# Optimization experiments

Measured on AMD Instinct MI355X. Metric: run time of the kernel, lower is better.

The kernel has to match this reference:

```python
import jax, jax.numpy as jnp
import numpy as np

FEAT_STRIDE = 16
SCALES = np.array([8.0, 16.0, 32.0])
RATIOS = np.array([0.5, 1.0, 2.0])
PRE_NMS_TOP_N = 6000
POST_NMS_TOP_N = 300
NMS_THRESH = 0.7


def _whctrs(anchor):
    w = anchor[2] - anchor[0] + 1.0
    h = anchor[3] - anchor[1] + 1.0
    cx = anchor[0] + 0.5 * (w - 1.0)
    cy = anchor[1] + 0.5 * (h - 1.0)
    return w, h, cx, cy


def _mkanchors(ws, hs, cx, cy):
    return np.stack([cx - 0.5 * (ws - 1.0), cy - 0.5 * (hs - 1.0),
                     cx + 0.5 * (ws - 1.0), cy + 0.5 * (hs - 1.0)], axis=1)


def generate_anchors(base_size=16, ratios=RATIOS, scales=SCALES):
    base = np.array([0.0, 0.0, base_size - 1.0, base_size - 1.0])
    w, h, cx, cy = _whctrs(base)
    size = w * h
    ws = np.round(np.sqrt(size / ratios))
    hs = np.round(ws * ratios)
    ratio_anchors = _mkanchors(ws, hs, cx, cy)
    out = []
    for a in ratio_anchors:
        w, h, cx, cy = _whctrs(a)
        out.append(_mkanchors(w * scales, h * scales, cx, cy))
    return np.vstack(out)  # (A=9, 4)


def setup_inputs():
    key = jax.random.key(0)
    k1, k2 = jax.random.split(key)
    B, A, H, W = 8, 9, 152, 152
    scores_in = jax.random.normal(k1, (B, 2 * A, H, W), jnp.float32)
    bbox_deltas = 0.5 * jax.random.normal(k2, (B, 4 * A, H, W), jnp.float32)
    im_info = jnp.tile(jnp.array([[H * FEAT_STRIDE, W * FEAT_STRIDE, 1.0]], jnp.float32), (B, 1))
    anchors = jnp.asarray(generate_anchors(), jnp.float32)
    return {"scores_in": scores_in, "bbox_deltas": bbox_deltas, "im_info": im_info, "anchors": anchors}


def bbox_transform_inv(boxes, deltas):
    w = boxes[..., 2] - boxes[..., 0] + 1.0
    h = boxes[..., 3] - boxes[..., 1] + 1.0
    cx = boxes[..., 0] + 0.5 * w
    cy = boxes[..., 1] + 0.5 * h
    dx, dy, dw, dh = deltas[..., 0], deltas[..., 1], deltas[..., 2], deltas[..., 3]
    pcx = dx * w + cx
    pcy = dy * h + cy
    pw = jnp.exp(dw) * w
    ph = jnp.exp(dh) * h
    return jnp.stack([pcx - 0.5 * pw, pcy - 0.5 * ph, pcx + 0.5 * pw, pcy + 0.5 * ph], axis=-1)


def clip_boxes(boxes, im_info):
    wmax = im_info[:, None, 1] - 1.0  # x bound, per image
    hmax = im_info[:, None, 0] - 1.0  # y bound
    x1 = jnp.minimum(jnp.maximum(boxes[..., 0], 0.0), wmax)
    y1 = jnp.minimum(jnp.maximum(boxes[..., 1], 0.0), hmax)
    x2 = jnp.minimum(jnp.maximum(boxes[..., 2], 0.0), wmax)
    y2 = jnp.minimum(jnp.maximum(boxes[..., 3], 0.0), hmax)
    return jnp.stack([x1, y1, x2, y2], axis=-1)


def nms_indices(boxes, thresh, max_out):
    # boxes: (N, 4), sorted by score descending. Greedy NMS -> up to max_out indices, -1 padded.
    x1, y1, x2, y2 = boxes[:, 0], boxes[:, 1], boxes[:, 2], boxes[:, 3]
    areas = (x2 - x1 + 1.0) * (y2 - y1 + 1.0)
    N = boxes.shape[0]

    def body(i, carry):
        suppressed, keep = carry
        idx = jnp.argmax(~suppressed)  # first surviving box = highest remaining score
        valid = ~suppressed[idx]
        keep = keep.at[i].set(jnp.where(valid, idx.astype(jnp.int32), -1))
        xx1 = jnp.maximum(x1[idx], x1)
        yy1 = jnp.maximum(y1[idx], y1)
        xx2 = jnp.minimum(x2[idx], x2)
        yy2 = jnp.minimum(y2[idx], y2)
        inter = jnp.maximum(xx2 - xx1 + 1.0, 0.0) * jnp.maximum(yy2 - yy1 + 1.0, 0.0)
        iou = inter / (areas[idx] + areas - inter)
        suppressed = jnp.where(valid, suppressed | (iou > thresh), suppressed)
        return suppressed, keep

    _, keep = jax.lax.fori_loop(0, max_out, body,
                                (jnp.zeros(N, bool), jnp.full(max_out, -1, jnp.int32)))
    return keep


def _forward(scores_in, bbox_deltas, im_info, anchors):
    B, _, H, W = scores_in.shape
    A = anchors.shape[0]
    # fg objectness scores: channels [A:2A] -> (B, K*A) in (row, col, anchor) order
    scores = scores_in[:, A:].transpose(0, 2, 3, 1).reshape(B, -1)
    deltas = bbox_deltas.transpose(0, 2, 3, 1).reshape(B, -1, 4)
    sx = (jnp.arange(W) * FEAT_STRIDE).astype(jnp.float32)
    sy = (jnp.arange(H) * FEAT_STRIDE).astype(jnp.float32)
    gx, gy = jnp.meshgrid(sx, sy)  # (H, W)
    shifts = jnp.stack([gx.ravel(), gy.ravel(), gx.ravel(), gy.ravel()], axis=1)  # (K, 4)
    all_anchors = (anchors[None, :, :] + shifts[:, None, :]).reshape(-1, 4)  # (K*A, 4)
    proposals = bbox_transform_inv(all_anchors[None], deltas)  # (B, K*A, 4)
    proposals = clip_boxes(proposals, im_info)
    _, order = jax.lax.top_k(scores, PRE_NMS_TOP_N)  # descending, == sorted order truncated
    props_top = jnp.take_along_axis(proposals, order[..., None], axis=1)  # (B, PRE, 4)
    keep = jax.vmap(lambda b: nms_indices(b, NMS_THRESH, POST_NMS_TOP_N))(props_top)  # (B, POST)
    valid = keep >= 0
    sel = jnp.take_along_axis(props_top, jnp.maximum(keep, 0)[..., None], axis=1)
    sel = jnp.where(valid[..., None], sel, 0.0)
    batch_col = jnp.broadcast_to(jnp.arange(B, dtype=jnp.float32)[:, None, None],
                                 (B, POST_NMS_TOP_N, 1))
    return jnp.concatenate([batch_col, sel], axis=2)  # (B, POST, 5)


def reference(scores_in, bbox_deltas, im_info, anchors):
    return _forward(scores_in, bbox_deltas, im_info, anchors)
```

## Files before the change

### kernel.cpp

```cpp
#include <hip/hip_runtime.h>
#include <stdint.h>

#define H_ 152
#define W_ 152
#define A_ 9
#define HW_ (H_ * W_)
#define N_ (HW_ * A_)
#define B_ 8
#define PRE_TOP 6000
#define POST_TOP 300
#define NBUCK 4096
#define NFINE 32768
#define CAND_CAP 8192
#define NMS_TH 0.7f
#define CNT_STRIDE 32
#define RTILE 512

#define OFF_HIST    0
#define OFF_SSUF    131072
#define OFF_CNT     262144
#define OFF_CAND    263168
#define OFF_GROUP   787456
#define OFF_BOXES   1311744
#define OFF_BALL    2079744
#define WS_NEED     (2079744ull + 26615808ull)


__device__ __forceinline__ unsigned fkey(float f) {
    unsigned u = __float_as_uint(f);
    return (u & 0x80000000u) ? ~u : (u | 0x80000000u);
}

__device__ __forceinline__ bool sup_test(float ax1, float ay1, float ax2, float ay2, float aar,
                                         float bx1, float by1, float bx2, float by2, float bar) {
    float xx1 = fmaxf(ax1, bx1);
    float yy1 = fmaxf(ay1, by1);
    float xx2 = fminf(ax2, bx2);
    float yy2 = fminf(ay2, by2);
    float iw = fmaxf(xx2 - xx1 + 1.0f, 0.0f);
    float ih = fmaxf(yy2 - yy1 + 1.0f, 0.0f);
    float inter = __fmul_rn(iw, ih);
    float iou = inter / (aar + bar - inter);
    return iou > NMS_TH;
}

__device__ __forceinline__ float4 decode_box(float an0, float an1, float an2, float an3,
                                             float sx, float sy,
                                             float dx, float dy, float dw, float dh,
                                             float wmax, float hmax) {
    float ax1 = an0 + sx;
    float ay1 = an1 + sy;
    float ax2 = an2 + sx;
    float ay2 = an3 + sy;
    float ww = ax2 - ax1 + 1.0f;
    float hh = ay2 - ay1 + 1.0f;
    float ctx = ax1 + 0.5f * ww;
    float cty = ay1 + 0.5f * hh;
    float pcx = __fadd_rn(__fmul_rn(dx, ww), ctx);
    float pcy = __fadd_rn(__fmul_rn(dy, hh), cty);
    float pw = __fmul_rn(expf(dw), ww);
    float ph = __fmul_rn(expf(dh), hh);
    float x1 = pcx - 0.5f * pw;
    float y1 = pcy - 0.5f * ph;
    float x2 = pcx + 0.5f * pw;
    float y2 = pcy + 0.5f * ph;
    x1 = fminf(fmaxf(x1, 0.0f), wmax);
    y1 = fminf(fmaxf(y1, 0.0f), hmax);
    x2 = fminf(fmaxf(x2, 0.0f), wmax);
    y2 = fminf(fmaxf(y2, 0.0f), hmax);
    return make_float4(x1, y1, x2, y2);
}


__global__ void zero2_k(unsigned* __restrict__ base, unsigned* __restrict__ p2) {
    const int n1 = 263168 / 4;
    const int n2 = 768000 / 4;
    int i = blockIdx.x * blockDim.x + threadIdx.x;
    int st = gridDim.x * blockDim.x;
    for (int k = i; k < n1 + n2; k += st) {
        if (k < n1) base[k] = 0u;
        else p2[k - n1] = 0u;
    }
}

__global__ void decode_all_k(const float* __restrict__ deltas,
                             const float* __restrict__ anchors,
                             const float* __restrict__ im_info,
                             float4* __restrict__ ball) {
    int ba = blockIdx.y;
    int b = ba / A_, a = ba - (ba / A_) * A_;
    int pix = blockIdx.x * blockDim.x + threadIdx.x;
    if (pix >= HW_) return;
    const float* db = deltas + ((size_t)b * 36 + 4 * a) * HW_;
    float dx = db[pix];
    float dy = db[pix + HW_];
    float dw = db[pix + 2 * HW_];
    float dh = db[pix + 3 * HW_];
    float an0 = anchors[a * 4 + 0];
    float an1 = anchors[a * 4 + 1];
    float an2 = anchors[a * 4 + 2];
    float an3 = anchors[a * 4 + 3];
    float hmax = im_info[b * 3 + 0] - 1.0f;
    float wmax = im_info[b * 3 + 1] - 1.0f;
    int w = pix % W_, h = pix / W_;
    float sx = (float)(w * 16), sy = (float)(h * 16);
    ball[(size_t)b * N_ + a * HW_ + pix] =
        decode_box(an0, an1, an2, an3, sx, sy, dx, dy, dw, dh, wmax, hmax);
}

__global__ void hist_k(const float* __restrict__ scores, unsigned* __restrict__ hist) {
    __shared__ unsigned lh[NBUCK];
    int b = blockIdx.y;
    for (int i = threadIdx.x; i < NBUCK; i += blockDim.x) lh[i] = 0;
    __syncthreads();
    const float4* sb = (const float4*)(scores + ((size_t)b * 18 + A_) * HW_);
    const int N4 = N_ / 4;
    int stride = gridDim.x * blockDim.x;
    for (int e = blockIdx.x * blockDim.x + threadIdx.x; e < N4; e += stride) {
        float4 v = sb[e];
        atomicAdd(&lh[fkey(v.x) >> 20], 1u);
        atomicAdd(&lh[fkey(v.y) >> 20], 1u);
        atomicAdd(&lh[fkey(v.z) >> 20], 1u);
        atomicAdd(&lh[fkey(v.w) >> 20], 1u);
    }
    __syncthreads();
    for (int i = threadIdx.x; i < NBUCK; i += blockDim.x) {
        unsigned v = lh[i];
        if (v) atomicAdd(&hist[b * NBUCK + i], v);
    }
}

__global__ void scan_k(const unsigned* __restrict__ hist, unsigned* __restrict__ bucketT) {
    __shared__ unsigned ps[1024];
    int b = blockIdx.x, t = threadIdx.x;
    const unsigned* hb = hist + b * NBUCK;
    unsigned c0 = hb[4095 - (4 * t + 0)];
    unsigned c1 = hb[4095 - (4 * t + 1)];
    unsigned c2 = hb[4095 - (4 * t + 2)];
    unsigned c3 = hb[4095 - (4 * t + 3)];
    unsigned local = c0 + c1 + c2 + c3;
    ps[t] = local;
    __syncthreads();
    for (int off = 1; off < 1024; off <<= 1) {
        unsigned v = (t >= off) ? ps[t - off] : 0u;
        __syncthreads();
        ps[t] += v;
        __syncthreads();
    }
    unsigned incl = ps[t], excl = incl - local;
    if (excl < PRE_TOP && incl >= PRE_TOP) {
        unsigned cum = excl;
        unsigned cc[4] = {c0, c1, c2, c3};
#pragma unroll
        for (int k = 0; k < 4; ++k) {
            cum += cc[k];
            if (cum >= PRE_TOP) { bucketT[b] = (unsigned)(4095 - (4 * t + k)); break; }
        }
    }
    if (t == 1023 && ps[1023] < PRE_TOP) bucketT[b] = 0;
}

__global__ void compact_k(const float* __restrict__ scores, const unsigned* __restrict__ bucketT,
                          unsigned* __restrict__ cnt, uint2* __restrict__ cand) {
    __shared__ unsigned wtot[4], wbase[4];
    __shared__ unsigned blkbase;
    int b = blockIdx.y;
    const float4* sb = (const float4*)(scores + ((size_t)b * 18 + A_) * HW_);
    unsigned T = bucketT[b];
    int lane = threadIdx.x & 63;
    int wid = threadIdx.x >> 6;
    const int N4 = N_ / 4;
    int stride = gridDim.x * blockDim.x;
    int niters = (N4 + stride - 1) / stride;
    unsigned long long lower = (lane == 63) ? 0x7fffffffffffffffull
                                            : ((1ull << lane) - 1ull);
    for (int it = 0; it < niters; ++it) {
        int e = it * stride + blockIdx.x * (int)blockDim.x + (int)threadIdx.x;
        bool p0 = false, p1 = false, p2 = false, p3 = false;
        unsigned k0 = 0, k1 = 0, k2 = 0, k3 = 0;
        if (e < N4) {
            float4 v = sb[e];
            k0 = fkey(v.x); k1 = fkey(v.y); k2 = fkey(v.z); k3 = fkey(v.w);
            p0 = (k0 >> 20) >= T; p1 = (k1 >> 20) >= T;
            p2 = (k2 >> 20) >= T; p3 = (k3 >> 20) >= T;
        }
        unsigned long long m0 = __ballot(p0), m1 = __ballot(p1);
        unsigned long long m2 = __ballot(p2), m3 = __ballot(p3);
        unsigned t0 = (unsigned)__popcll(m0), t1 = (unsigned)__popcll(m1);
        unsigned t2 = (unsigned)__popcll(m2), t3 = (unsigned)__popcll(m3);
        unsigned wtotal = t0 + t1 + t2 + t3;
        if (lane == 0) wtot[wid] = wtotal;
        __syncthreads();
        if (threadIdx.x == 0) {
            unsigned s0 = wtot[0], s1 = wtot[1], s2 = wtot[2], s3 = wtot[3];
            unsigned tot = s0 + s1 + s2 + s3;
            blkbase = tot ? atomicAdd(&cnt[b * CNT_STRIDE], tot) : 0u;
            wbase[0] = 0; wbase[1] = s0; wbase[2] = s0 + s1; wbase[3] = s0 + s1 + s2;
        }
        __syncthreads();
        if (wtotal) {
            unsigned base = blkbase + wbase[wid];
            unsigned o0 = base + (unsigned)__popcll(m0 & lower);
            unsigned o1 = base + t0 + (unsigned)__popcll(m1 & lower);
            unsigned o2 = base + t0 + t1 + (unsigned)__popcll(m2 & lower);
            unsigned o3 = base + t0 + t1 + t2 + (unsigned)__popcll(m3 & lower);
            uint2* cb = cand + (size_t)b * CAND_CAP;
            int e4 = e * 4;
            if (p0 && o0 < CAND_CAP) {
                int a = (e4 + 0) / HW_, pix = (e4 + 0) - a * HW_;
                cb[o0] = make_uint2(k0, (unsigned)(pix * A_ + a));
            }
            if (p1 && o1 < CAND_CAP) {
                int a = (e4 + 1) / HW_, pix = (e4 + 1) - a * HW_;
                cb[o1] = make_uint2(k1, (unsigned)(pix * A_ + a));
            }
            if (p2 && o2 < CAND_CAP) {
                int a = (e4 + 2) / HW_, pix = (e4 + 2) - a * HW_;
                cb[o2] = make_uint2(k2, (unsigned)(pix * A_ + a));
            }
            if (p3 && o3 < CAND_CAP) {
                int a = (e4 + 3) / HW_, pix = (e4 + 3) - a * HW_;
                cb[o3] = make_uint2(k3, (unsigned)(pix * A_ + a));
            }
        }
    }
}

__global__ void __launch_bounds__(1024) finesort_k(const unsigned* __restrict__ cnt,
                                                   uint2* __restrict__ cand,
                                                   unsigned long long* __restrict__ grouped) {
    __shared__ unsigned lh[NFINE];
    __shared__ unsigned ps[1024];
    int b = blockIdx.x, t = threadIdx.x;
    int M = min((int)cnt[b * CNT_STRIDE], CAND_CAP);
    uint2* cb = cand + (size_t)b * CAND_CAP;
    unsigned long long* g = grouped + (size_t)b * CAND_CAP;
    for (int i = t; i < NFINE; i += 1024) lh[i] = 0u;
    __syncthreads();
    for (int i = t; i < M; i += 1024) {
        unsigned key16 = cb[i].x >> 16;
        unsigned f = (key16 >= 32768u) ? (key16 - 32768u) : 0u;
        atomicAdd(&lh[f], 1u);
    }
    __syncthreads();
    unsigned c[32];
    unsigned local = 0;
#pragma unroll
    for (int k = 0; k < 32; ++k) { c[k] = lh[32767 - (32 * t + k)]; local += c[k]; }
    ps[t] = local;
    __syncthreads();
    for (int off = 1; off < 1024; off <<= 1) {
        unsigned v = (t >= off) ? ps[t - off] : 0u;
        __syncthreads();
        ps[t] += v;
        __syncthreads();
    }
    unsigned run = ps[t] - local;
    __syncthreads();
#pragma unroll
    for (int k = 0; k < 32; ++k) {
        lh[32767 - (32 * t + k)] = run;
        run += c[k];
    }
    __syncthreads();
    for (int i = t; i < M; i += 1024) {
        uint2 cd = cb[i];
        unsigned key16 = cd.x >> 16;
        unsigned f = (key16 >= 32768u) ? (key16 - 32768u) : 0u;
        unsigned pos = atomicAdd(&lh[f], 1u);
        if (pos < CAND_CAP)
            g[pos] = ((unsigned long long)cd.x << 32) | (unsigned)(~cd.y);
    }
    __syncthreads();
    ushort* S16 = (ushort*)cb;
    for (int i = t; i < NFINE; i += 1024)
        S16[i] = (ushort)min(lh[i], 65535u);
}

__global__ void __launch_bounds__(256) rank_k(const unsigned* __restrict__ cnt,
                                              const unsigned long long* __restrict__ grouped,
                                              const ushort* __restrict__ S16all,
                                              const float* __restrict__ deltas,
                                              const float* __restrict__ anchors,
                                              const float* __restrict__ im_info,
                                              const float4* __restrict__ ball,
                                              float4* __restrict__ boxes) {
    __shared__ unsigned long long tile[RTILE];
    __shared__ int s_rs, s_re;
    int b = blockIdx.y, t = threadIdx.x;
    int M = min((int)cnt[b * CNT_STRIDE], CAND_CAP);
    int c0 = blockIdx.x * 256;
    if (c0 >= M) return;
    const unsigned long long* g = grouped + (size_t)b * CAND_CAP;
    const ushort* S16 = S16all + (size_t)b * NFINE;
    int i = c0 + t;
    bool valid = i < M;
    unsigned long long comp = valid ? g[i] : 0ull;

    unsigned n = valid ? ~(unsigned)comp : 0u;
    int a = (int)(n % A_);
    int pix = (int)(n / A_);

    float4 pre = make_float4(0.f, 0.f, 0.f, 0.f);
    float dx = 0.f, dy = 0.f, dw = 0.f, dh = 0.f;
    float an0 = 0.f, an1 = 0.f, an2 = 0.f, an3 = 0.f, hmax = 0.f, wmax = 0.f;
    if (ball) {
        if (valid) pre = ball[(size_t)b * N_ + a * HW_ + pix];
    } else if (valid) {
        const float* db = deltas + (size_t)b * 36 * HW_;
        int didx = (4 * a) * HW_ + pix;
        dx = db[didx];
        dy = db[didx + HW_];
        dw = db[didx + 2 * HW_];
        dh = db[didx + 3 * HW_];
        an0 = anchors[a * 4 + 0];
        an1 = anchors[a * 4 + 1];
        an2 = anchors[a * 4 + 2];
        an3 = anchors[a * 4 + 3];
        hmax = im_info[b * 3 + 0] - 1.0f;
        wmax = im_info[b * 3 + 1] - 1.0f;
    }

    unsigned key16 = (unsigned)(comp >> 48);
    int f = (key16 >= 32768u) ? (int)(key16 - 32768u) : 0;
    int bs = 0, be = 0;
    if (valid) {
        bs = (f < 32767) ? min((int)S16[f + 1], M) : 0;
        be = min((int)S16[f], M);
    }
    if (t == 0) {
        unsigned kf = (unsigned)(g[c0] >> 48);
        int bf = (kf >= 32768u) ? (int)(kf - 32768u) : 0;
        int last = min(c0 + 255, M - 1);
        unsigned kl = (unsigned)(g[last] >> 48);
        int bl = (kl >= 32768u) ? (int)(kl - 32768u) : 0;
        s_rs = (bf < 32767) ? min((int)S16[bf + 1], M) : 0;
        s_re = min((int)S16[bl], M);
    }
    __syncthreads();
    int rs = s_rs, re = s_re;
    int cgt = 0;
    for (int tb = rs; tb < re; tb += RTILE) {
        int navail = min(RTILE, re - tb);
        __syncthreads();
        for (int j = t; j < navail; j += 256) tile[j] = g[tb + j];
        __syncthreads();
        if (valid) {
            int lo = max(bs, tb) - tb;
            int hi = min(be, tb + navail) - tb;
            int a0 = 0, a1 = 0, a2 = 0, a3 = 0, a4 = 0, a5 = 0, a6 = 0, a7 = 0;
            int j = lo;
            for (; j + 8 <= hi; j += 8) {
                unsigned long long v0 = tile[j + 0];
                unsigned long long v1 = tile[j + 1];
                unsigned long long v2 = tile[j + 2];
                unsigned long long v3 = tile[j + 3];
                unsigned long long v4 = tile[j + 4];
                unsigned long long v5 = tile[j + 5];
                unsigned long long v6 = tile[j + 6];
                unsigned long long v7 = tile[j + 7];
                a0 += (v0 > comp); a1 += (v1 > comp); a2 += (v2 > comp); a3 += (v3 > comp);
                a4 += (v4 > comp); a5 += (v5 > comp); a6 += (v6 > comp); a7 += (v7 > comp);
            }
            for (; j < hi; ++j) cgt += (tile[j] > comp);
            cgt += (a0 + a1 + a2 + a3) + (a4 + a5 + a6 + a7);
        }
    }
    if (!valid) return;
    int rank = bs + cgt;
    if (rank >= PRE_TOP) return;

    float4 result;
    if (ball) {
        result = pre;
    } else {
        int w = pix % W_, h = pix / W_;
        float sx = (float)(w * 16), sy = (float)(h * 16);
        result = decode_box(an0, an1, an2, an3, sx, sy, dx, dy, dw, dh, wmax, hmax);
    }
    boxes[(size_t)b * PRE_TOP + rank] = result;
}

__global__ void __launch_bounds__(1024) nms_k(const float4* __restrict__ boxes,
                                              float* __restrict__ out) {
    __shared__ float kx1[POST_TOP], ky1[POST_TOP], kx2[POST_TOP], ky2[POST_TOP], kar[POST_TOP];
    __shared__ float gx1[64], gy1[64], gx2[64], gy2[64], gar[64];
    __shared__ unsigned extw[2];
    __shared__ unsigned intraw[128];
    __shared__ unsigned long long s_keep;
    __shared__ int s_base, s_kc, s_done;
    int b = blockIdx.x, t = threadIdx.x;
    if (t == 0) { s_kc = 0; s_done = 0; }
    const float4* bb = boxes + (size_t)b * PRE_TOP;
    const int ngroups = (PRE_TOP + 63) / 64;

    float4 vcur = make_float4(0.f, 0.f, 0.f, 0.f);
    if (t < 64) vcur = bb[t];

    for (int g = 0; g < ngroups; ++g) {
        __syncthreads();
        if (s_done) break;
        int gbase = g * 64;
        int gsz = min(64, PRE_TOP - gbase);
        if (t < gsz) {
            gx1[t] = vcur.x; gy1[t] = vcur.y; gx2[t] = vcur.z; gy2[t] = vcur.w;
            gar[t] = __fmul_rn(vcur.z - vcur.x + 1.0f, vcur.w - vcur.y + 1.0f);
        }
        if (t < 64) {
            int nidx = min(gbase + 64 + t, PRE_TOP - 1);
            vcur = bb[nidx];
        }
        if (t < 2) extw[t] = 0u;
        if (t < 128) intraw[t] = 0u;
        __syncthreads();

        int kc = s_kc;
        {
            int j = t >> 4, sub = t & 15;
            if (j < gsz) {
                float ax1 = gx1[j], ay1 = gy1[j], ax2 = gx2[j], ay2 = gy2[j], aar = gar[j];
                bool any = false;
                for (int kk = sub; kk < kc; kk += 16) {
                    if (sup_test(kx1[kk], ky1[kk], kx2[kk], ky2[kk], kar[kk],
                                 ax1, ay1, ax2, ay2, aar)) { any = true; break; }
                }
                if (any) atomicOr(&extw[j >> 5], 1u << (j & 31));
            }
        }
        for (int p = t; p < 4096; p += 1024) {
            int jj = p >> 6, ll = p & 63;
            if (jj < ll && ll < gsz) {
                if (sup_test(gx1[jj], gy1[jj], gx2[jj], gy2[jj], gar[jj],
                             gx1[ll], gy1[ll], gx2[ll], gy2[ll], gar[ll])) {
                    atomicOr(&intraw[2 * jj + (ll >> 5)], 1u << (ll & 31));
                }
            }
        }
        __syncthreads();

        if (t == 0) {
            unsigned long long ext64 = (unsigned long long)extw[0] |
                                       ((unsigned long long)extw[1] << 32);
            unsigned long long valid = (gsz >= 64) ? ~0ull : ((1ull << gsz) - 1ull);
            unsigned long long alive = (~ext64) & valid;
            unsigned long long keep = 0ull;
            int kcc = s_kc;
            s_base = kcc;
            while (alive && kcc < POST_TOP) {
                int j = __ffsll((long long)alive) - 1;
                keep |= (1ull << j);
                ++kcc;
                unsigned long long row = (unsigned long long)intraw[2 * j] |
                                         ((unsigned long long)intraw[2 * j + 1] << 32);
                alive &= ~row;
                alive &= ~(1ull << j);
            }
            s_keep = keep;
            s_kc = kcc;
            if (kcc >= POST_TOP) s_done = 1;
        }
        __syncthreads();

        if (t < gsz && ((s_keep >> t) & 1ull)) {
            int rank = __popcll(s_keep & ((1ull << t) - 1ull));
            int slot = s_base + rank;
            kx1[slot] = gx1[t]; ky1[slot] = gy1[t];
            kx2[slot] = gx2[t]; ky2[slot] = gy2[t]; kar[slot] = gar[t];
            float* o = out + (size_t)(b * POST_TOP + slot) * 5;
            o[0] = (float)b; o[1] = gx1[t]; o[2] = gy1[t]; o[3] = gx2[t]; o[4] = gy2[t];
        }
    }
    __syncthreads();
    for (int sl = s_kc + t; sl < POST_TOP; sl += 1024) {
        float* o = out + (size_t)(b * POST_TOP + sl) * 5;
        o[0] = (float)b; o[1] = 0.f; o[2] = 0.f; o[3] = 0.f; o[4] = 0.f;
    }
}


extern "C" void kernel_launch(void* const* d_in, const int* in_sizes, int n_in,
                              void* d_out, int out_size, void* d_ws, size_t ws_size,
                              hipStream_t stream) {
    const float* scores  = (const float*)d_in[0];
    const float* deltas  = (const float*)d_in[1];
    const float* im_info = (const float*)d_in[2];
    const float* anchors = (const float*)d_in[3];
    float* out = (float*)d_out;

    unsigned*           hist    = (unsigned*)((char*)d_ws + OFF_HIST);
    unsigned*           cnt     = (unsigned*)((char*)d_ws + OFF_CNT);
    uint2*              cand    = (uint2*)((char*)d_ws + OFF_CAND);
    unsigned long long* grouped = (unsigned long long*)((char*)d_ws + OFF_GROUP);
    float4*             boxes   = (float4*)((char*)d_ws + OFF_BOXES);
    unsigned*           bucketT = cnt + B_ * CNT_STRIDE - 8;

    bool useBall = ws_size >= WS_NEED;
    float4* ball = useBall ? (float4*)((char*)d_ws + OFF_BALL) : nullptr;

    zero2_k<<<256, 256, 0, stream>>>((unsigned*)d_ws, (unsigned*)((char*)d_ws + OFF_BOXES));
    if (useBall) {
        decode_all_k<<<dim3((HW_ + 255) / 256, B_ * A_), 256, 0, stream>>>(
            deltas, anchors, im_info, ball);
    }
    hist_k<<<dim3(64, B_), 256, 0, stream>>>(scores, hist);
    scan_k<<<B_, 1024, 0, stream>>>(hist, bucketT);
    compact_k<<<dim3(64, B_), 256, 0, stream>>>(scores, bucketT, cnt, cand);
    finesort_k<<<B_, 1024, 0, stream>>>(cnt, cand, grouped);
    rank_k<<<dim3(32, B_), 256, 0, stream>>>(cnt, grouped, (const ushort*)cand,
                                             deltas, anchors, im_info, ball, boxes);
    nms_k<<<B_, 1024, 0, stream>>>(boxes, out);
}
```

Measured before the change: 99.16 us.

## Fuse zero and decode kernels; ballot-based intra-group NMS mask with float4 LDS

Merges the workspace zeroing kernel and the full-anchor decode kernel into one launch, with block ranges split between the two jobs, so one kernel launch and its gap go away. In NMS, boxes are stored as float4 in LDS, and the intra-group suppression matrix is built with wave ballots. That replaces one atomicOr per suppressed pair with at most two per row. The fused kernel runs with a fixed zeroing block count, which may change how the two jobs overlap.

Result: faster. 93.59 us (-5.6%).

```diff
diff --git a/kernel.cpp b/kernel.cpp
--- a/kernel.cpp
+++ b/kernel.cpp
@@ -15,6 +15,9 @@
 #define NMS_TH 0.7f
 #define CNT_STRIDE 32
 #define RTILE 512
+#define DEC_PIXBLK 91
+#define DEC_BLKS (72 * DEC_PIXBLK)
+#define ZERO_BLKS 128
 
 #define OFF_HIST    0
 #define OFF_SSUF    131072
@@ -72,40 +75,43 @@
 }
 
 
-__global__ void zero2_k(unsigned* __restrict__ base, unsigned* __restrict__ p2) {
-    const int n1 = 263168 / 4;
-    const int n2 = 768000 / 4;
-    int i = blockIdx.x * blockDim.x + threadIdx.x;
-    int st = gridDim.x * blockDim.x;
-    for (int k = i; k < n1 + n2; k += st) {
-        if (k < n1) base[k] = 0u;
-        else p2[k - n1] = 0u;
-    }
-}
-
-__global__ void decode_all_k(const float* __restrict__ deltas,
-                             const float* __restrict__ anchors,
-                             const float* __restrict__ im_info,
-                             float4* __restrict__ ball) {
-    int ba = blockIdx.y;
-    int b = ba / A_, a = ba - (ba / A_) * A_;
-    int pix = blockIdx.x * blockDim.x + threadIdx.x;
-    if (pix >= HW_) return;
-    const float* db = deltas + ((size_t)b * 36 + 4 * a) * HW_;
-    float dx = db[pix];
-    float dy = db[pix + HW_];
-    float dw = db[pix + 2 * HW_];
-    float dh = db[pix + 3 * HW_];
-    float an0 = anchors[a * 4 + 0];
-    float an1 = anchors[a * 4 + 1];
-    float an2 = anchors[a * 4 + 2];
-    float an3 = anchors[a * 4 + 3];
-    float hmax = im_info[b * 3 + 0] - 1.0f;
-    float wmax = im_info[b * 3 + 1] - 1.0f;
-    int w = pix % W_, h = pix / W_;
-    float sx = (float)(w * 16), sy = (float)(h * 16);
-    ball[(size_t)b * N_ + a * HW_ + pix] =
-        decode_box(an0, an1, an2, an3, sx, sy, dx, dy, dw, dh, wmax, hmax);
+__global__ void init_k(const float* __restrict__ deltas,
+                       const float* __restrict__ anchors,
+                       const float* __restrict__ im_info,
+                       float4* __restrict__ ball,
+                       unsigned* __restrict__ zbase, unsigned* __restrict__ zboxes,
+                       int nDecBlks) {
+    int bid = blockIdx.x;
+    if (bid < nDecBlks) {
+        int ba = bid / DEC_PIXBLK;
+        int b = ba / A_, a = ba - (ba / A_) * A_;
+        int pix = (bid % DEC_PIXBLK) * 256 + threadIdx.x;
+        if (pix >= HW_) return;
+        const float* db = deltas + ((size_t)b * 36 + 4 * a) * HW_;
+        float dx = db[pix];
+        float dy = db[pix + HW_];
+        float dw = db[pix + 2 * HW_];
+        float dh = db[pix + 3 * HW_];
+        float an0 = anchors[a * 4 + 0];
+        float an1 = anchors[a * 4 + 1];
+        float an2 = anchors[a * 4 + 2];
+        float an3 = anchors[a * 4 + 3];
+        float hmax = im_info[b * 3 + 0] - 1.0f;
+        float wmax = im_info[b * 3 + 1] - 1.0f;
+        int w = pix % W_, h = pix / W_;
+        float sx = (float)(w * 16), sy = (float)(h * 16);
+        ball[(size_t)b * N_ + a * HW_ + pix] =
+            decode_box(an0, an1, an2, an3, sx, sy, dx, dy, dw, dh, wmax, hmax);
+    } else {
+        const int n1 = 263168 / 4;
+        const int n2 = 768000 / 4;
+        int i = (bid - nDecBlks) * 256 + (int)threadIdx.x;
+        int st = ZERO_BLKS * 256;
+        for (int k = i; k < n1 + n2; k += st) {
+            if (k < n1) zbase[k] = 0u;
+            else zboxes[k - n1] = 0u;
+        }
+    }
 }
 
 __global__ void hist_k(const float* __restrict__ scores, unsigned* __restrict__ hist) {
@@ -383,13 +389,16 @@
 
 __global__ void __launch_bounds__(1024) nms_k(const float4* __restrict__ boxes,
                                               float* __restrict__ out) {
-    __shared__ float kx1[POST_TOP], ky1[POST_TOP], kx2[POST_TOP], ky2[POST_TOP], kar[POST_TOP];
-    __shared__ float gx1[64], gy1[64], gx2[64], gy2[64], gar[64];
+    __shared__ float4 kbox[POST_TOP];
+    __shared__ float  karea[POST_TOP];
+    __shared__ float4 gbox4[64];
+    __shared__ float  gar[64];
     __shared__ unsigned extw[2];
     __shared__ unsigned intraw[128];
     __shared__ unsigned long long s_keep;
     __shared__ int s_base, s_kc, s_done;
     int b = blockIdx.x, t = threadIdx.x;
+    int lane = t & 63, w = t >> 6;
     if (t == 0) { s_kc = 0; s_done = 0; }
     const float4* bb = boxes + (size_t)b * PRE_TOP;
     const int ngroups = (PRE_TOP + 63) / 64;
@@ -403,7 +412,7 @@
         int gbase = g * 64;
         int gsz = min(64, PRE_TOP - gbase);
         if (t < gsz) {
-            gx1[t] = vcur.x; gy1[t] = vcur.y; gx2[t] = vcur.z; gy2[t] = vcur.w;
+            gbox4[t] = vcur;
             gar[t] = __fmul_rn(vcur.z - vcur.x + 1.0f, vcur.w - vcur.y + 1.0f);
         }
         if (t < 64) {
@@ -418,22 +427,33 @@
         {
             int j = t >> 4, sub = t & 15;
             if (j < gsz) {
-                float ax1 = gx1[j], ay1 = gy1[j], ax2 = gx2[j], ay2 = gy2[j], aar = gar[j];
+                float4 cb4 = gbox4[j];
+                float car = gar[j];
                 bool any = false;
-                for (int kk = sub; kk < kc; kk += 16) {
-                    if (sup_test(kx1[kk], ky1[kk], kx2[kk], ky2[kk], kar[kk],
-                                 ax1, ay1, ax2, ay2, aar)) { any = true; break; }
+                for (int kk = sub; kk < kc && !any; kk += 16) {
+                    float4 kb = kbox[kk];
+                    float ka = karea[kk];
+                    any = sup_test(kb.x, kb.y, kb.z, kb.w, ka,
+                                   cb4.x, cb4.y, cb4.z, cb4.w, car);
                 }
                 if (any) atomicOr(&extw[j >> 5], 1u << (j & 31));
             }
         }
-        for (int p = t; p < 4096; p += 1024) {
-            int jj = p >> 6, ll = p & 63;
-            if (jj < ll && ll < gsz) {
-                if (sup_test(gx1[jj], gy1[jj], gx2[jj], gy2[jj], gar[jj],
-                             gx1[ll], gy1[ll], gx2[ll], gy2[ll], gar[ll])) {
-                    atomicOr(&intraw[2 * jj + (ll >> 5)], 1u << (ll & 31));
-                }
+        {
+            float4 mb = gbox4[lane];
+            float mar = gar[lane];
+#pragma unroll
+            for (int it = 0; it < 4; ++it) {
+                int jj = w + it * 16;
+                float4 bj = gbox4[jj];
+                float baj = gar[jj];
+                bool sup = (jj < lane) && (lane < gsz) && (jj < gsz) &&
+                           sup_test(bj.x, bj.y, bj.z, bj.w, baj,
+                                    mb.x, mb.y, mb.z, mb.w, mar);
+                unsigned long long m = __ballot(sup);
+                if (lane == 0 && (unsigned)m) atomicOr(&intraw[2 * jj], (unsigned)m);
+                if (lane == 1 && (unsigned)(m >> 32))
+                    atomicOr(&intraw[2 * jj + 1], (unsigned)(m >> 32));
             }
         }
         __syncthreads();
@@ -441,8 +461,8 @@
         if (t == 0) {
             unsigned long long ext64 = (unsigned long long)extw[0] |
                                        ((unsigned long long)extw[1] << 32);
-            unsigned long long valid = (gsz >= 64) ? ~0ull : ((1ull << gsz) - 1ull);
-            unsigned long long alive = (~ext64) & valid;
+            unsigned long long validm = (gsz >= 64) ? ~0ull : ((1ull << gsz) - 1ull);
+            unsigned long long alive = (~ext64) & validm;
             unsigned long long keep = 0ull;
             int kcc = s_kc;
             s_base = kcc;
@@ -464,10 +484,11 @@
         if (t < gsz && ((s_keep >> t) & 1ull)) {
             int rank = __popcll(s_keep & ((1ull << t) - 1ull));
             int slot = s_base + rank;
-            kx1[slot] = gx1[t]; ky1[slot] = gy1[t];
-            kx2[slot] = gx2[t]; ky2[slot] = gy2[t]; kar[slot] = gar[t];
+            float4 mb = gbox4[t];
+            kbox[slot] = mb;
+            karea[slot] = gar[t];
             float* o = out + (size_t)(b * POST_TOP + slot) * 5;
-            o[0] = (float)b; o[1] = gx1[t]; o[2] = gy1[t]; o[3] = gx2[t]; o[4] = gy2[t];
+            o[0] = (float)b; o[1] = mb.x; o[2] = mb.y; o[3] = mb.z; o[4] = mb.w;
         }
     }
     __syncthreads();
@@ -497,11 +518,10 @@
     bool useBall = ws_size >= WS_NEED;
     float4* ball = useBall ? (float4*)((char*)d_ws + OFF_BALL) : nullptr;
 
-    zero2_k<<<256, 256, 0, stream>>>((unsigned*)d_ws, (unsigned*)((char*)d_ws + OFF_BOXES));
-    if (useBall) {
-        decode_all_k<<<dim3((HW_ + 255) / 256, B_ * A_), 256, 0, stream>>>(
-            deltas, anchors, im_info, ball);
-    }
+    int nDec = useBall ? DEC_BLKS : 0;
+    init_k<<<nDec + ZERO_BLKS, 256, 0, stream>>>(deltas, anchors, im_info, ball,
+                                                 (unsigned*)d_ws,
+                                                 (unsigned*)((char*)d_ws + OFF_BOXES), nDec);
     hist_k<<<dim3(64, B_), 256, 0, stream>>>(scores, hist);
     scan_k<<<B_, 1024, 0, stream>>>(hist, bucketT);
     compact_k<<<dim3(64, B_), 256, 0, stream>>>(scores, bucketT, cnt, cand);
```
